# Kernel optimization log

Measured on AMD Instinct MI355X. Metric: run time of the kernel, lower is better.

Reference implementation:

```python
import jax, jax.numpy as jnp
import numpy as np

EPS = 1e-5
B, C1, C2, H, W = 8, 256, 256, 80, 80
C_ = C2 // 2
K = 3

def _bn(x, g, b, m, v):
    # inference-mode BatchNorm with given affine params / running stats
    return g * (x - m) * jax.lax.rsqrt(v + EPS) + b

def setup_inputs():
    key = jax.random.key(0)
    ks = jax.random.split(key, 18)
    rn = jax.random.normal
    ru = jax.random.uniform
    inp = {}
    inp['x'] = rn(ks[0], (B, C1, H, W), jnp.float32)
    # cv1: 1x1 conv (no bias) + BN
    inp['W1'] = rn(ks[1], (C_, C1), jnp.float32) * 0.05
    inp['g1'] = 1.0 + 0.1 * rn(ks[2], (C_,), jnp.float32)
    inp['b1'] = 0.1 * rn(ks[3], (C_,), jnp.float32)
    inp['m1'] = 0.1 * rn(ks[4], (C_,), jnp.float32)
    inp['v1'] = 0.5 + ru(ks[5], (C_,), jnp.float32)
    # RFAConv.get_weights: grouped 1x1 conv (groups=C_, 9->9 per group, with bias) + BN
    inp['Wg'] = rn(ks[6], (C_, K * K, K * K), jnp.float32) * 0.2
    inp['bg'] = 0.1 * rn(ks[7], (C_, K * K), jnp.float32)
    inp['gg'] = 1.0 + 0.1 * rn(ks[8], (C_, K * K), jnp.float32)
    inp['bgw'] = 0.1 * rn(ks[9], (C_, K * K), jnp.float32)
    inp['mg'] = 0.1 * rn(ks[10], (C_, K * K), jnp.float32)
    inp['vg'] = 0.5 + ru(ks[11], (C_, K * K), jnp.float32)
    # RFAConv.conv: kernel-3 stride-3 conv flattened to [C2, C_, 9], with bias; + BN
    inp['Wc'] = rn(ks[12], (C2, C_, K * K), jnp.float32) * 0.03
    inp['bc'] = 0.1 * rn(ks[13], (C2,), jnp.float32)
    inp['g2'] = 1.0 + 0.1 * rn(ks[14], (C2,), jnp.float32)
    inp['b2'] = 0.1 * rn(ks[15], (C2,), jnp.float32)
    inp['m2'] = 0.1 * rn(ks[16], (C2,), jnp.float32)
    inp['v2'] = 0.5 + ru(ks[17], (C2,), jnp.float32)
    return inp

def reference(x, W1, g1, b1, m1, v1, Wg, bg, gg, bgw, mg, vg, Wc, bc, g2, b2, m2, v2):
    # cv1: 1x1 conv + BN + SiLU
    h = jnp.einsum('oc,bchw->bohw', W1, x)
    h = _bn(h, g1[:, None, None], b1[:, None, None], m1[:, None, None], v1[:, None, None])
    h = jax.nn.silu(h)
    # nn.Unfold(k=3, pad=1): patches[b, c, n, y, x] with n = i*3 + j (torch layout)
    hp = jnp.pad(h, ((0, 0), (0, 0), (1, 1), (1, 1)))
    patches = jnp.stack([hp[:, :, i:i + H, j:j + W] for i in range(K) for j in range(K)], axis=2)  # [B,C_,9,H,W]
    # grouped 1x1 conv (per-channel 9->9 mixing) + BN + softmax over receptive field
    w = jnp.einsum('coi,bcihw->bcohw', Wg, patches) + bg[:, :, None, None]
    w = _bn(w, gg[:, :, None, None], bgw[:, :, None, None], mg[:, :, None, None], vg[:, :, None, None])
    w = jax.nn.softmax(w, axis=2)
    # weighted receptive-field data; stride-3 kernel-3 conv over the block-expanded
    # (3H,3W) layout reduces exactly to a contraction over (channel, kernel-index)
    out = jnp.einsum('ocn,bcnhw->bohw', Wc, patches * w) + bc[:, None, None]
    out = _bn(out, g2[:, None, None], b2[:, None, None], m2[:, None, None], v2[:, None, None])
    out = jax.nn.relu(out)
    return x + out
```

## Files before the change

kernel.cpp:

```cpp
#include <hip/hip_runtime.h>
#include <hip/hip_bf16.h>

#define B_   8
#define C1_  256
#define C2_  256
#define Cm_  128
#define H_   80
#define W_   80
#define HW_  6400
#define CN_  1152
#define EPS_ 1e-5f

typedef __attribute__((ext_vector_type(8))) short bf16x8;
typedef __attribute__((ext_vector_type(4))) float f32x4;

__device__ inline unsigned short f2bf(float f) {
  union { float f; unsigned int u; } v; v.f = f;
  unsigned int u = v.u;
  unsigned int r = (u + 0x7FFFu + ((u >> 16) & 1u)) >> 16;
  return (unsigned short)r;
}
__device__ inline float bf2f(unsigned short s) {
  union { unsigned int u; float f; } v; v.u = ((unsigned int)s) << 16;
  return v.f;
}

__device__ __forceinline__ void gload16(const void* g, void* l) {
  __builtin_amdgcn_global_load_lds(
      (const __attribute__((address_space(1))) void*)g,
      (__attribute__((address_space(3))) void*)l, 16, 0, 0);
}

__global__ __launch_bounds__(256) void k0_prep(
    const float* __restrict__ Wc, const float* __restrict__ bc,
    const float* __restrict__ g2, const float* __restrict__ b2,
    const float* __restrict__ m2, const float* __restrict__ v2,
    const float* __restrict__ Wg, const float* __restrict__ bg,
    const float* __restrict__ gg, const float* __restrict__ bgw,
    const float* __restrict__ mg, const float* __restrict__ vg,
    const float* __restrict__ W1,
    unsigned short* __restrict__ Wcb, float* __restrict__ A2,
    float* __restrict__ B2, float* __restrict__ Wgt,
    float* __restrict__ bgt, unsigned short* __restrict__ W1b) {
  int idx = blockIdx.x * 256 + threadIdx.x;
  if (idx < C2_ * CN_) {
    int o = idx / CN_;
    int r = idx - o * CN_;
    int n = r >> 7;
    int c = r & 127;
    Wcb[idx] = f2bf(Wc[o * CN_ + c * 9 + n]);
  }
  if (idx < Cm_ * 81) {
    int c  = idx / 81;
    int oi = idx - c * 81;
    int n  = oi / 9;
    float sg = gg[c * 9 + n] * rsqrtf(vg[c * 9 + n] + EPS_);
    Wgt[oi * 128 + c] = Wg[idx] * sg;
  }
  if (idx < Cm_ * 9) {
    int c = idx / 9;
    int n = idx - c * 9;
    float sg = gg[idx] * rsqrtf(vg[idx] + EPS_);
    bgt[n * 128 + c] = (bg[idx] - mg[idx]) * sg + bgw[idx];
  }
  if (idx < Cm_ * C1_) W1b[idx] = f2bf(W1[idx]);
  if (idx < C2_) {
    float s = g2[idx] * rsqrtf(v2[idx] + EPS_);
    A2[idx] = s;
    B2[idx] = (bc[idx] - m2[idx]) * s + b2[idx];
  }
}

__global__ __launch_bounds__(256) void k1_cv1(
    const float* __restrict__ x, const unsigned short* __restrict__ W1b,
    const float* __restrict__ g1, const float* __restrict__ b1,
    const float* __restrict__ m1, const float* __restrict__ v1,
    unsigned short* __restrict__ h) {
  __shared__ alignas(16) unsigned short Ash[2][128 * 64];
  __shared__ alignas(16) unsigned short Bsh[2][64 * 64];

  const int b   = blockIdx.y;
  const int hw0 = blockIdx.x * 64;
  const int t   = threadIdx.x;
  const int w   = __builtin_amdgcn_readfirstlane(t >> 6);
  const int l15 = t & 15;
  const int lhi = (t & 63) >> 4;

  const char* W1B = (const char*)W1b;
  int aoffs[4], aldsb[4];
#pragma unroll
  for (int j = 0; j < 4; ++j) {
    int L16  = j * 256 + t;
    int row  = L16 >> 3;
    int colb = (L16 & 7) * 16;
    aoffs[j] = row * (C1_ * 2) + (colb ^ ((row & 7) << 4));
    aldsb[j] = L16 * 16;
  }
  const int c_l = t & 63;
  const int px0 = (t >> 6) * 16;

#define STAGEA(BUF, KC)                                                        \
  _Pragma("unroll") for (int j = 0; j < 4; ++j)                                \
      gload16(W1B + aoffs[j] + (KC) * 128, (char*)&Ash[BUF][0] + aldsb[j]);
#define LOADB(KC)                                                              \
  _Pragma("unroll") for (int u = 0; u < 4; ++u)                                \
      xv[u] = *reinterpret_cast<const float4*>(                                \
          x + ((size_t)(b * C1_ + (KC) * 64 + c_l)) * HW_ + hw0 + px0 + u * 4);
#define WRITEB(BUF)                                                            \
  _Pragma("unroll") for (int u = 0; u < 4; ++u)                                \
    _Pragma("unroll") for (int e = 0; e < 4; ++e) {                            \
      int px = px0 + u * 4 + e;                                                \
      float vv = (e == 0) ? xv[u].x : (e == 1) ? xv[u].y                       \
               : (e == 2) ? xv[u].z : xv[u].w;                                 \
      Bsh[BUF][px * 64 + (c_l ^ (((u * 4 + e) & 7) << 3))] = f2bf(vv);         \
    }

  f32x4 acc[2][4];
#pragma unroll
  for (int i = 0; i < 2; ++i)
#pragma unroll
    for (int nf = 0; nf < 4; ++nf) acc[i][nf] = (f32x4)0.f;

  const int swzs = (l15 & 7) << 3;
  const int lhi8 = lhi * 8;

  float4 xv[4];
  STAGEA(0, 0);
  LOADB(0);
  WRITEB(0);
  __syncthreads();

  int cur = 0;
  for (int kc = 0; kc < 4; ++kc) {
    if (kc < 3) {
      STAGEA(cur ^ 1, kc + 1);
      LOADB(kc + 1);
    }
    const unsigned short* Ab = &Ash[cur][0];
    const unsigned short* Bb = &Bsh[cur][0];
#pragma unroll
    for (int ks = 0; ks < 2; ++ks) {
      bf16x8 av[2], bv[4];
#pragma unroll
      for (int mf = 0; mf < 2; ++mf) {
        int row = w * 32 + mf * 16 + l15;
        av[mf] = *reinterpret_cast<const bf16x8*>(
            Ab + row * 64 + (((ks << 5) + lhi8) ^ swzs));
      }
#pragma unroll
      for (int nf = 0; nf < 4; ++nf) {
        int row = nf * 16 + l15;
        bv[nf] = *reinterpret_cast<const bf16x8*>(
            Bb + row * 64 + (((ks << 5) + lhi8) ^ swzs));
      }
#pragma unroll
      for (int mf = 0; mf < 2; ++mf)
#pragma unroll
        for (int nf = 0; nf < 4; ++nf)
          acc[mf][nf] = __builtin_amdgcn_mfma_f32_16x16x32_bf16(
              av[mf], bv[nf], acc[mf][nf], 0, 0, 0);
    }
    if (kc < 3) WRITEB(cur ^ 1);
    __syncthreads();
    cur ^= 1;
  }
#undef STAGEA
#undef LOADB
#undef WRITEB

#pragma unroll
  for (int mf = 0; mf < 2; ++mf) {
#pragma unroll
    for (int r = 0; r < 4; ++r) {
      int o = w * 32 + mf * 16 + lhi * 4 + r;
      float s  = g1[o] * rsqrtf(v1[o] + EPS_);
      float sh = b1[o] - m1[o] * s;
#pragma unroll
      for (int nf = 0; nf < 4; ++nf) {
        float val = fmaf(acc[mf][nf][r], s, sh);
        float sig = 1.f / (1.f + __expf(-val));
        h[((size_t)b * Cm_ + o) * HW_ + hw0 + nf * 16 + l15] = f2bf(val * sig);
      }
    }
  }
}

__global__ __launch_bounds__(256) void k2a_weights(
    const unsigned short* __restrict__ h,
    const float* __restrict__ Wgt, const float* __restrict__ bgt,
    unsigned short* __restrict__ vt) {
  __shared__ unsigned short ht[Cm_ * 30];
  __shared__ unsigned short vbuf[8][CN_];

  const int b  = blockIdx.z;
  const int y  = blockIdx.y;
  const int x0 = blockIdx.x * 8;
  const int t  = threadIdx.x;

  for (int idx = t; idx < Cm_ * 30; idx += 256) {
    int c   = idx / 30;
    int rem = idx - c * 30;
    int r   = rem / 10;
    int xx  = rem - r * 10;
    int gy  = y + r - 1;
    int gx  = x0 + xx - 1;
    unsigned short val = 0;
    if ((unsigned)gy < (unsigned)H_ && (unsigned)gx < (unsigned)W_)
      val = h[((size_t)b * Cm_ + c) * HW_ + gy * W_ + gx];
    ht[idx] = val;
  }
  __syncthreads();

  const int c  = t & 127;
  const int p0 = t >> 7;

  float p[4][9];
  {
    float f[3][10];
#pragma unroll
    for (int r = 0; r < 3; ++r) {
      const unsigned int* src =
          reinterpret_cast<const unsigned int*>(&ht[c * 30 + r * 10]);
#pragma unroll
      for (int u = 0; u < 5; ++u) {
        unsigned int d = src[u];
        f[r][2 * u]     = bf2f((unsigned short)(d & 0xffffu));
        f[r][2 * u + 1] = bf2f((unsigned short)(d >> 16));
      }
    }
#pragma unroll
    for (int j = 0; j < 4; ++j)
#pragma unroll
      for (int r = 0; r < 3; ++r)
#pragma unroll
        for (int cc = 0; cc < 3; ++cc)
          p[j][r * 3 + cc] = p0 ? f[r][2 * j + 1 + cc] : f[r][2 * j + cc];
  }

  float wv[9][4];
#pragma unroll
  for (int n = 0; n < 9; ++n) {
    float bgv = bgt[n * 128 + c];
    float wg[9];
#pragma unroll
    for (int i = 0; i < 9; ++i) wg[i] = Wgt[(n * 9 + i) * 128 + c];
#pragma unroll
    for (int j = 0; j < 4; ++j) {
      float a = bgv;
#pragma unroll
      for (int i = 0; i < 9; ++i) a = fmaf(wg[i], p[j][i], a);
      wv[n][j] = a;
    }
  }

#pragma unroll
  for (int j = 0; j < 4; ++j) {
    int px = p0 + 2 * j;
    float mx = wv[0][j];
#pragma unroll
    for (int n = 1; n < 9; ++n) mx = fmaxf(mx, wv[n][j]);
    float e[9], sum = 0.f;
#pragma unroll
    for (int n = 0; n < 9; ++n) { e[n] = __expf(wv[n][j] - mx); sum += e[n]; }
    float inv = 1.f / sum;
#pragma unroll
    for (int n = 0; n < 9; ++n)
      vbuf[px][n * 128 + c] = f2bf(p[j][n] * e[n] * inv);
  }
  __syncthreads();

  for (int idx = t; idx < 8 * (CN_ / 8); idx += 256) {
    int px  = idx / 144;
    int off = idx - px * 144;
    const uint4* src = reinterpret_cast<const uint4*>(&vbuf[px][off * 8]);
    int hw = y * W_ + x0 + px;
    uint4* dst = reinterpret_cast<uint4*>(vt + ((size_t)b * HW_ + hw) * CN_ + off * 8);
    *dst = *src;
  }
}

__global__ __launch_bounds__(512, 4) void k2b_gemm(
    const unsigned short* __restrict__ Wcb, const unsigned short* __restrict__ vt,
    const float* __restrict__ A2, const float* __restrict__ B2,
    const float* __restrict__ x, float* __restrict__ out) {
  __shared__ alignas(16) unsigned short Ash[2][256 * 64];
  __shared__ alignas(16) unsigned short Bsh[2][64 * 64];

  const int b   = blockIdx.y;
  const int n0  = blockIdx.x * 64;
  const int t   = threadIdx.x;
  const int w   = __builtin_amdgcn_readfirstlane(t >> 6);
  const int l   = t & 63;
  const int l15 = l & 15;
  const int lhi = l >> 4;
  const int mw  = w >> 1;
  const int nw  = w & 1;

  const char* WcbB = (const char*)Wcb;
  const char* vtB  = (const char*)vt;
  int  aoffs[4], aldsb[4];
#pragma unroll
  for (int j = 0; j < 4; ++j) {
    int L16  = (w * 4 + j) * 64 + l;
    int row  = L16 >> 3;
    int colb = (L16 & 7) * 16;
    aoffs[j] = row * (CN_ * 2) + (colb ^ ((row & 7) << 4));
    aldsb[j] = L16 * 16;
  }
  const int bpx  = t >> 3;
  const long boff = (long)((size_t)(b * HW_ + n0 + bpx) * CN_) * 2 +
                    (((t & 7) * 16) ^ ((bpx & 7) << 4));
  const int bldsb = t * 16;

#define STAGE(BUF, TT) do {                                                    \
    _Pragma("unroll") for (int j = 0; j < 4; ++j)                              \
      gload16(WcbB + aoffs[j] + (TT) * 128, (char*)&Ash[BUF][0] + aldsb[j]);   \
    gload16(vtB + boff + (TT) * 128, (char*)&Bsh[BUF][0] + bldsb);             \
  } while (0)

  f32x4 acc[4][2];
#pragma unroll
  for (int i = 0; i < 4; ++i)
#pragma unroll
    for (int nf = 0; nf < 2; ++nf) acc[i][nf] = (f32x4)0.f;

  const int swzs = (l15 & 7) << 3;
  const int lhi8 = lhi * 8;

  STAGE(0, 0);
  __syncthreads();

  int cur = 0;
  for (int tt = 0; tt < 18; ++tt) {
    if (tt < 17) STAGE(cur ^ 1, tt + 1);
    const unsigned short* Ab = &Ash[cur][0];
    const unsigned short* Bb = &Bsh[cur][0];
#pragma unroll
    for (int ks = 0; ks < 2; ++ks) {
      bf16x8 av[4], bv[2];
#pragma unroll
      for (int mf = 0; mf < 4; ++mf) {
        int row = mw * 64 + mf * 16 + l15;
        av[mf] = *reinterpret_cast<const bf16x8*>(
            Ab + row * 64 + (((ks << 5) + lhi8) ^ swzs));
      }
#pragma unroll
      for (int nf = 0; nf < 2; ++nf) {
        int row = nw * 32 + nf * 16 + l15;
        bv[nf] = *reinterpret_cast<const bf16x8*>(
            Bb + row * 64 + (((ks << 5) + lhi8) ^ swzs));
      }
#pragma unroll
      for (int mf = 0; mf < 4; ++mf)
#pragma unroll
        for (int nf = 0; nf < 2; ++nf)
          acc[mf][nf] = __builtin_amdgcn_mfma_f32_16x16x32_bf16(
              av[mf], bv[nf], acc[mf][nf], 0, 0, 0);
    }
    __syncthreads();
    cur ^= 1;
  }
#undef STAGE

#pragma unroll
  for (int mf = 0; mf < 4; ++mf) {
#pragma unroll
    for (int r = 0; r < 4; ++r) {
      int o = mw * 64 + mf * 16 + lhi * 4 + r;
      float sA = A2[o], sB = B2[o];
#pragma unroll
      for (int nf = 0; nf < 2; ++nf) {
        float val = fmaf(acc[mf][nf][r], sA, sB);
        val = fmaxf(val, 0.f);
        size_t idx = ((size_t)b * C2_ + o) * HW_ + n0 + nw * 32 + nf * 16 + l15;
        out[idx] = x[idx] + val;
      }
    }
  }
}

extern "C" void kernel_launch(void* const* d_in, const int* in_sizes, int n_in,
                              void* d_out, int out_size, void* d_ws, size_t ws_size,
                              hipStream_t stream) {
  (void)in_sizes; (void)n_in; (void)out_size; (void)ws_size;
  const float* x   = (const float*)d_in[0];
  const float* W1  = (const float*)d_in[1];
  const float* g1  = (const float*)d_in[2];
  const float* b1  = (const float*)d_in[3];
  const float* m1  = (const float*)d_in[4];
  const float* v1  = (const float*)d_in[5];
  const float* Wg  = (const float*)d_in[6];
  const float* bg  = (const float*)d_in[7];
  const float* gg  = (const float*)d_in[8];
  const float* bgw = (const float*)d_in[9];
  const float* mg  = (const float*)d_in[10];
  const float* vg  = (const float*)d_in[11];
  const float* Wc  = (const float*)d_in[12];
  const float* bc  = (const float*)d_in[13];
  const float* g2  = (const float*)d_in[14];
  const float* b2  = (const float*)d_in[15];
  const float* m2  = (const float*)d_in[16];
  const float* v2  = (const float*)d_in[17];
  float* outp = (float*)d_out;

  char* ws = (char*)d_ws;
  unsigned short* h   = (unsigned short*)ws;
  unsigned short* vt  = (unsigned short*)(ws + 13107200);
  unsigned short* Wcb = (unsigned short*)(ws + 131072000);
  float*          Wgt = (float*)(ws + 131661824);
  float*          bgt = (float*)(ws + 131703296);
  float*          A2  = (float*)(ws + 131707904);
  float*          B2  = A2 + C2_;
  unsigned short* W1b = (unsigned short*)(ws + 131709952);

  k0_prep<<<dim3((C2_ * CN_ + 255) / 256), 256, 0, stream>>>(
      Wc, bc, g2, b2, m2, v2, Wg, bg, gg, bgw, mg, vg, W1,
      Wcb, A2, B2, Wgt, bgt, W1b);

  dim3 grid1(HW_ / 64, B_);
  k1_cv1<<<grid1, 256, 0, stream>>>(x, W1b, g1, b1, m1, v1, h);

  dim3 grid2a(W_ / 8, H_, B_);
  k2a_weights<<<grid2a, 256, 0, stream>>>(h, Wgt, bgt, vt);

  dim3 grid2b(HW_ / 64, B_);
  k2b_gemm<<<grid2b, 512, 0, stream>>>(Wcb, vt, A2, B2, x, outp);
}
```

Before: 152.7 us.

## Fuse receptive-field attention weighting into the output GEMM, removing vt intermediate

Merges the softmax-weighting kernel and the output GEMM into one kernel. Each block handles 40 pixels of one row, computes the weighted patches for 32-channel chunks into shared memory, and immediately runs MFMAs against Wc read directly from global memory. This removes the roughly 118 MB bf16 vt round-trip through HBM, and Wc is now used in its natural (c, n) ordering. The cost is that A operands are no longer staged through LDS. Using 48 N-columns for 40 pixels wastes some MFMA work, and the vbuf layout may cause LDS bank conflicts.

New measurement: 232.4 us. +52.3%, slower.

```diff
diff --git a/kernel.cpp b/kernel.cpp
--- a/kernel.cpp
+++ b/kernel.cpp
@@ -10,6 +10,12 @@
 #define HW_  6400
 #define CN_  1152
 #define EPS_ 1e-5f
+
+#define CH_   32
+#define NCHK_ 4
+#define KCH_  288
+#define NPX_  40
+#define VSTR_ 296
 
 typedef __attribute__((ext_vector_type(8))) short bf16x8;
 typedef __attribute__((ext_vector_type(4))) float f32x4;
@@ -43,13 +49,7 @@
     float* __restrict__ B2, float* __restrict__ Wgt,
     float* __restrict__ bgt, unsigned short* __restrict__ W1b) {
   int idx = blockIdx.x * 256 + threadIdx.x;
-  if (idx < C2_ * CN_) {
-    int o = idx / CN_;
-    int r = idx - o * CN_;
-    int n = r >> 7;
-    int c = r & 127;
-    Wcb[idx] = f2bf(Wc[o * CN_ + c * 9 + n]);
-  }
+  if (idx < C2_ * CN_) Wcb[idx] = f2bf(Wc[idx]);
   if (idx < Cm_ * 81) {
     int c  = idx / 81;
     int oi = idx - c * 81;
@@ -185,195 +185,134 @@
   }
 }
 
-__global__ __launch_bounds__(256) void k2a_weights(
+__global__ __launch_bounds__(256, 2) void k2f(
     const unsigned short* __restrict__ h,
     const float* __restrict__ Wgt, const float* __restrict__ bgt,
-    unsigned short* __restrict__ vt) {
-  __shared__ unsigned short ht[Cm_ * 30];
-  __shared__ unsigned short vbuf[8][CN_];
-
-  const int b  = blockIdx.z;
-  const int y  = blockIdx.y;
-  const int x0 = blockIdx.x * 8;
-  const int t  = threadIdx.x;
-
-  for (int idx = t; idx < Cm_ * 30; idx += 256) {
-    int c   = idx / 30;
-    int rem = idx - c * 30;
-    int r   = rem / 10;
-    int xx  = rem - r * 10;
-    int gy  = y + r - 1;
-    int gx  = x0 + xx - 1;
-    unsigned short val = 0;
-    if ((unsigned)gy < (unsigned)H_ && (unsigned)gx < (unsigned)W_)
-      val = h[((size_t)b * Cm_ + c) * HW_ + gy * W_ + gx];
-    ht[idx] = val;
-  }
-  __syncthreads();
-
-  const int c  = t & 127;
-  const int p0 = t >> 7;
-
-  float p[4][9];
-  {
-    float f[3][10];
-#pragma unroll
-    for (int r = 0; r < 3; ++r) {
-      const unsigned int* src =
-          reinterpret_cast<const unsigned int*>(&ht[c * 30 + r * 10]);
-#pragma unroll
-      for (int u = 0; u < 5; ++u) {
-        unsigned int d = src[u];
-        f[r][2 * u]     = bf2f((unsigned short)(d & 0xffffu));
-        f[r][2 * u + 1] = bf2f((unsigned short)(d >> 16));
-      }
-    }
-#pragma unroll
-    for (int j = 0; j < 4; ++j)
-#pragma unroll
-      for (int r = 0; r < 3; ++r)
-#pragma unroll
-        for (int cc = 0; cc < 3; ++cc)
-          p[j][r * 3 + cc] = p0 ? f[r][2 * j + 1 + cc] : f[r][2 * j + cc];
-  }
-
-  float wv[9][4];
-#pragma unroll
-  for (int n = 0; n < 9; ++n) {
-    float bgv = bgt[n * 128 + c];
-    float wg[9];
-#pragma unroll
-    for (int i = 0; i < 9; ++i) wg[i] = Wgt[(n * 9 + i) * 128 + c];
-#pragma unroll
-    for (int j = 0; j < 4; ++j) {
-      float a = bgv;
-#pragma unroll
-      for (int i = 0; i < 9; ++i) a = fmaf(wg[i], p[j][i], a);
-      wv[n][j] = a;
-    }
-  }
-
-#pragma unroll
-  for (int j = 0; j < 4; ++j) {
-    int px = p0 + 2 * j;
-    float mx = wv[0][j];
-#pragma unroll
-    for (int n = 1; n < 9; ++n) mx = fmaxf(mx, wv[n][j]);
-    float e[9], sum = 0.f;
-#pragma unroll
-    for (int n = 0; n < 9; ++n) { e[n] = __expf(wv[n][j] - mx); sum += e[n]; }
-    float inv = 1.f / sum;
-#pragma unroll
-    for (int n = 0; n < 9; ++n)
-      vbuf[px][n * 128 + c] = f2bf(p[j][n] * e[n] * inv);
-  }
-  __syncthreads();
-
-  for (int idx = t; idx < 8 * (CN_ / 8); idx += 256) {
-    int px  = idx / 144;
-    int off = idx - px * 144;
-    const uint4* src = reinterpret_cast<const uint4*>(&vbuf[px][off * 8]);
-    int hw = y * W_ + x0 + px;
-    uint4* dst = reinterpret_cast<uint4*>(vt + ((size_t)b * HW_ + hw) * CN_ + off * 8);
-    *dst = *src;
-  }
-}
-
-__global__ __launch_bounds__(512, 4) void k2b_gemm(
-    const unsigned short* __restrict__ Wcb, const unsigned short* __restrict__ vt,
+    const unsigned short* __restrict__ Wcb,
     const float* __restrict__ A2, const float* __restrict__ B2,
     const float* __restrict__ x, float* __restrict__ out) {
-  __shared__ alignas(16) unsigned short Ash[2][256 * 64];
-  __shared__ alignas(16) unsigned short Bsh[2][64 * 64];
-
-  const int b   = blockIdx.y;
-  const int n0  = blockIdx.x * 64;
-  const int t   = threadIdx.x;
-  const int w   = __builtin_amdgcn_readfirstlane(t >> 6);
-  const int l   = t & 63;
-  const int l15 = l & 15;
-  const int lhi = l >> 4;
-  const int mw  = w >> 1;
-  const int nw  = w & 1;
-
-  const char* WcbB = (const char*)Wcb;
-  const char* vtB  = (const char*)vt;
-  int  aoffs[4], aldsb[4];
-#pragma unroll
-  for (int j = 0; j < 4; ++j) {
-    int L16  = (w * 4 + j) * 64 + l;
-    int row  = L16 >> 3;
-    int colb = (L16 & 7) * 16;
-    aoffs[j] = row * (CN_ * 2) + (colb ^ ((row & 7) << 4));
-    aldsb[j] = L16 * 16;
-  }
-  const int bpx  = t >> 3;
-  const long boff = (long)((size_t)(b * HW_ + n0 + bpx) * CN_) * 2 +
-                    (((t & 7) * 16) ^ ((bpx & 7) << 4));
-  const int bldsb = t * 16;
-
-#define STAGE(BUF, TT) do {                                                    \
-    _Pragma("unroll") for (int j = 0; j < 4; ++j)                              \
-      gload16(WcbB + aoffs[j] + (TT) * 128, (char*)&Ash[BUF][0] + aldsb[j]);   \
-    gload16(vtB + boff + (TT) * 128, (char*)&Bsh[BUF][0] + bldsb);             \
-  } while (0)
-
-  f32x4 acc[4][2];
-#pragma unroll
-  for (int i = 0; i < 4; ++i)
-#pragma unroll
-    for (int nf = 0; nf < 2; ++nf) acc[i][nf] = (f32x4)0.f;
-
-  const int swzs = (l15 & 7) << 3;
-  const int lhi8 = lhi * 8;
-
-  STAGE(0, 0);
-  __syncthreads();
-
-  int cur = 0;
-  for (int tt = 0; tt < 18; ++tt) {
-    if (tt < 17) STAGE(cur ^ 1, tt + 1);
-    const unsigned short* Ab = &Ash[cur][0];
-    const unsigned short* Bb = &Bsh[cur][0];
-#pragma unroll
-    for (int ks = 0; ks < 2; ++ks) {
-      bf16x8 av[4], bv[2];
-#pragma unroll
-      for (int mf = 0; mf < 4; ++mf) {
-        int row = mw * 64 + mf * 16 + l15;
+  __shared__ unsigned short ht[CH_ * 3 * 42];
+  __shared__ alignas(16) unsigned short vbuf[48 * VSTR_];
+
+  const int half = blockIdx.x;
+  const int y    = blockIdx.y;
+  const int b    = blockIdx.z;
+  const int x0   = half * NPX_;
+  const int t    = threadIdx.x;
+  const int w    = __builtin_amdgcn_readfirstlane(t >> 6);
+  const int l15  = t & 15;
+  const int lhi  = (t & 63) >> 4;
+
+  const int c_l = t & 31;
+  const int pxg = t >> 5;
+
+  f32x4 acc[4][3];
+#pragma unroll
+  for (int mf = 0; mf < 4; ++mf)
+#pragma unroll
+    for (int nf = 0; nf < 3; ++nf) acc[mf][nf] = (f32x4)0.f;
+
+  for (int ch = 0; ch < NCHK_; ++ch) {
+#pragma unroll
+    for (int i = 0; i < 16; ++i) {
+      int idx = t + i * 256;
+      if (idx < CH_ * 3 * 42) {
+        int c   = idx / 126;
+        int rem = idx - c * 126;
+        int r   = rem / 42;
+        int xx  = rem - r * 42;
+        int gy  = y + r - 1;
+        int gx  = x0 + xx - 1;
+        unsigned short v = 0;
+        if ((unsigned)gy < (unsigned)H_ && (unsigned)gx < (unsigned)W_)
+          v = h[((size_t)b * Cm_ + ch * CH_ + c) * HW_ + gy * W_ + gx];
+        ht[idx] = v;
+      }
+    }
+    __syncthreads();
+
+    {
+      float f[3][7];
+      const int fb = c_l * 126 + pxg * 5;
+#pragma unroll
+      for (int r = 0; r < 3; ++r)
+#pragma unroll
+        for (int q = 0; q < 7; ++q)
+          f[r][q] = bf2f(ht[fb + r * 42 + q]);
+
+      const int cg = ch * CH_ + c_l;
+      float wv[9][5];
+#pragma unroll
+      for (int n = 0; n < 9; ++n) {
+        float bias = bgt[n * 128 + cg];
+        float wg[9];
+#pragma unroll
+        for (int i = 0; i < 9; ++i) wg[i] = Wgt[(n * 9 + i) * 128 + cg];
+#pragma unroll
+        for (int j = 0; j < 5; ++j) {
+          float a = bias;
+#pragma unroll
+          for (int ri = 0; ri < 3; ++ri)
+#pragma unroll
+            for (int ci = 0; ci < 3; ++ci)
+              a = fmaf(wg[ri * 3 + ci], f[ri][j + ci], a);
+          wv[n][j] = a;
+        }
+      }
+#pragma unroll
+      for (int j = 0; j < 5; ++j) {
+        float mx = wv[0][j];
+#pragma unroll
+        for (int n = 1; n < 9; ++n) mx = fmaxf(mx, wv[n][j]);
+        float e[9], sum = 0.f;
+#pragma unroll
+        for (int n = 0; n < 9; ++n) { e[n] = __expf(wv[n][j] - mx); sum += e[n]; }
+        float inv = 1.f / sum;
+        int vb = (pxg * 5 + j) * VSTR_ + c_l * 9;
+#pragma unroll
+        for (int n = 0; n < 9; ++n)
+          vbuf[vb + n] = f2bf(f[n / 3][j + n % 3] * e[n] * inv);
+      }
+    }
+    __syncthreads();
+
+#pragma unroll
+    for (int ks = 0; ks < 9; ++ks) {
+      bf16x8 av[4], bv[3];
+#pragma unroll
+      for (int mf = 0; mf < 4; ++mf)
         av[mf] = *reinterpret_cast<const bf16x8*>(
-            Ab + row * 64 + (((ks << 5) + lhi8) ^ swzs));
-      }
-#pragma unroll
-      for (int nf = 0; nf < 2; ++nf) {
-        int row = nw * 32 + nf * 16 + l15;
+            Wcb + (size_t)(w * 64 + mf * 16 + l15) * CN_ +
+            ch * KCH_ + ks * 32 + lhi * 8);
+#pragma unroll
+      for (int nf = 0; nf < 3; ++nf)
         bv[nf] = *reinterpret_cast<const bf16x8*>(
-            Bb + row * 64 + (((ks << 5) + lhi8) ^ swzs));
-      }
+            vbuf + (nf * 16 + l15) * VSTR_ + ks * 32 + lhi * 8);
 #pragma unroll
       for (int mf = 0; mf < 4; ++mf)
 #pragma unroll
-        for (int nf = 0; nf < 2; ++nf)
+        for (int nf = 0; nf < 3; ++nf)
           acc[mf][nf] = __builtin_amdgcn_mfma_f32_16x16x32_bf16(
               av[mf], bv[nf], acc[mf][nf], 0, 0, 0);
     }
     __syncthreads();
-    cur ^= 1;
-  }
-#undef STAGE
+  }
 
 #pragma unroll
   for (int mf = 0; mf < 4; ++mf) {
 #pragma unroll
     for (int r = 0; r < 4; ++r) {
-      int o = mw * 64 + mf * 16 + lhi * 4 + r;
+      int o = w * 64 + mf * 16 + lhi * 4 + r;
       float sA = A2[o], sB = B2[o];
 #pragma unroll
-      for (int nf = 0; nf < 2; ++nf) {
-        float val = fmaf(acc[mf][nf][r], sA, sB);
-        val = fmaxf(val, 0.f);
-        size_t idx = ((size_t)b * C2_ + o) * HW_ + n0 + nw * 32 + nf * 16 + l15;
-        out[idx] = x[idx] + val;
+      for (int nf = 0; nf < 3; ++nf) {
+        int px = nf * 16 + l15;
+        if (px < NPX_) {
+          float val = fmaf(acc[mf][nf][r], sA, sB);
+          val = fmaxf(val, 0.f);
+          size_t idx = ((size_t)b * C2_ + o) * HW_ + y * W_ + x0 + px;
+          out[idx] = x[idx] + val;
+        }
       }
     }
   }
@@ -405,13 +344,12 @@
 
   char* ws = (char*)d_ws;
   unsigned short* h   = (unsigned short*)ws;
-  unsigned short* vt  = (unsigned short*)(ws + 13107200);
-  unsigned short* Wcb = (unsigned short*)(ws + 131072000);
-  float*          Wgt = (float*)(ws + 131661824);
-  float*          bgt = (float*)(ws + 131703296);
-  float*          A2  = (float*)(ws + 131707904);
+  unsigned short* Wcb = (unsigned short*)(ws + 13107200);
+  float*          Wgt = (float*)(ws + 13697024);
+  float*          bgt = (float*)(ws + 13738496);
+  float*          A2  = (float*)(ws + 13743104);
   float*          B2  = A2 + C2_;
-  unsigned short* W1b = (unsigned short*)(ws + 131709952);
+  unsigned short* W1b = (unsigned short*)(ws + 13745152);
 
   k0_prep<<<dim3((C2_ * CN_ + 255) / 256), 256, 0, stream>>>(
       Wc, bc, g2, b2, m2, v2, Wg, bg, gg, bgw, mg, vg, W1,
@@ -420,9 +358,6 @@
   dim3 grid1(HW_ / 64, B_);
   k1_cv1<<<grid1, 256, 0, stream>>>(x, W1b, g1, b1, m1, v1, h);
 
-  dim3 grid2a(W_ / 8, H_, B_);
-  k2a_weights<<<grid2a, 256, 0, stream>>>(h, Wgt, bgt, vt);
-
-  dim3 grid2b(HW_ / 64, B_);
-  k2b_gemm<<<grid2b, 512, 0, stream>>>(Wcb, vt, A2, B2, x, outp);
-}
+  dim3 grid2(2, H_, B_);
+  k2f<<<grid2, 256, 0, stream>>>(h, Wgt, bgt, Wcb, A2, B2, x, outp);
+}
```

## Write softmax-weighted patches directly to global, drop LDS staging buffer

Applied to the files above, without the earlier changes.

The weights kernel now gives each thread two adjacent channels and two pixels instead of one channel and four pixels. Weights and biases are read as float2, and the bf16-packed results are stored straight to global memory as 32-bit words. This removes the vbuf shared staging array, one barrier and the 16-byte copy-out loop, which cuts LDS usage and may raise occupancy. In exchange the global stores become 4-byte writes rather than 16-byte vector stores, and rounding now goes through the HIP bf16 intrinsic.

New measurement: 184.3 us. 20.7% more time.

```diff
diff --git a/kernel.cpp b/kernel.cpp
--- a/kernel.cpp
+++ b/kernel.cpp
@@ -23,6 +23,11 @@
 __device__ inline float bf2f(unsigned short s) {
   union { unsigned int u; float f; } v; v.u = ((unsigned int)s) << 16;
   return v.f;
+}
+__device__ inline unsigned short bfb(float f) {
+  __hip_bfloat16 b = __float2bfloat16(f);
+  union { __hip_bfloat16 b; unsigned short u; } v; v.b = b;
+  return v.u;
 }
 
 __device__ __forceinline__ void gload16(const void* g, void* l) {
@@ -190,7 +195,6 @@
     const float* __restrict__ Wgt, const float* __restrict__ bgt,
     unsigned short* __restrict__ vt) {
   __shared__ unsigned short ht[Cm_ * 30];
-  __shared__ unsigned short vbuf[8][CN_];
 
   const int b  = blockIdx.z;
   const int y  = blockIdx.y;
@@ -211,71 +215,71 @@
   }
   __syncthreads();
 
-  const int c  = t & 127;
-  const int p0 = t >> 7;
-
-  float p[4][9];
-  {
-    float f[3][10];
+  const int cp = t & 63;
+  const int pp = t >> 6;
+
+  float f[2][3][4];
+#pragma unroll
+  for (int ch = 0; ch < 2; ++ch) {
+    int c = cp * 2 + ch;
 #pragma unroll
     for (int r = 0; r < 3; ++r) {
       const unsigned int* src =
-          reinterpret_cast<const unsigned int*>(&ht[c * 30 + r * 10]);
-#pragma unroll
-      for (int u = 0; u < 5; ++u) {
-        unsigned int d = src[u];
-        f[r][2 * u]     = bf2f((unsigned short)(d & 0xffffu));
-        f[r][2 * u + 1] = bf2f((unsigned short)(d >> 16));
-      }
-    }
-#pragma unroll
-    for (int j = 0; j < 4; ++j)
-#pragma unroll
-      for (int r = 0; r < 3; ++r)
-#pragma unroll
-        for (int cc = 0; cc < 3; ++cc)
-          p[j][r * 3 + cc] = p0 ? f[r][2 * j + 1 + cc] : f[r][2 * j + cc];
-  }
-
-  float wv[9][4];
+          reinterpret_cast<const unsigned int*>(&ht[c * 30 + r * 10]) + pp;
+      unsigned int d0 = src[0], d1 = src[1];
+      f[ch][r][0] = bf2f((unsigned short)(d0 & 0xffffu));
+      f[ch][r][1] = bf2f((unsigned short)(d0 >> 16));
+      f[ch][r][2] = bf2f((unsigned short)(d1 & 0xffffu));
+      f[ch][r][3] = bf2f((unsigned short)(d1 >> 16));
+    }
+  }
+
+  const float2* Wg2 = (const float2*)Wgt;
+  const float2* bg2 = (const float2*)bgt;
+
+  float wv[9][2][2];
 #pragma unroll
   for (int n = 0; n < 9; ++n) {
-    float bgv = bgt[n * 128 + c];
-    float wg[9];
-#pragma unroll
-    for (int i = 0; i < 9; ++i) wg[i] = Wgt[(n * 9 + i) * 128 + c];
-#pragma unroll
-    for (int j = 0; j < 4; ++j) {
-      float a = bgv;
-#pragma unroll
-      for (int i = 0; i < 9; ++i) a = fmaf(wg[i], p[j][i], a);
-      wv[n][j] = a;
-    }
-  }
-
-#pragma unroll
-  for (int j = 0; j < 4; ++j) {
-    int px = p0 + 2 * j;
-    float mx = wv[0][j];
-#pragma unroll
-    for (int n = 1; n < 9; ++n) mx = fmaxf(mx, wv[n][j]);
-    float e[9], sum = 0.f;
-#pragma unroll
-    for (int n = 0; n < 9; ++n) { e[n] = __expf(wv[n][j] - mx); sum += e[n]; }
-    float inv = 1.f / sum;
-#pragma unroll
-    for (int n = 0; n < 9; ++n)
-      vbuf[px][n * 128 + c] = f2bf(p[j][n] * e[n] * inv);
-  }
-  __syncthreads();
-
-  for (int idx = t; idx < 8 * (CN_ / 8); idx += 256) {
-    int px  = idx / 144;
-    int off = idx - px * 144;
-    const uint4* src = reinterpret_cast<const uint4*>(&vbuf[px][off * 8]);
-    int hw = y * W_ + x0 + px;
-    uint4* dst = reinterpret_cast<uint4*>(vt + ((size_t)b * HW_ + hw) * CN_ + off * 8);
-    *dst = *src;
+    float2 bias = bg2[n * 64 + cp];
+    float a00 = bias.x, a01 = bias.x, a10 = bias.y, a11 = bias.y;
+#pragma unroll
+    for (int ri = 0; ri < 3; ++ri)
+#pragma unroll
+      for (int ci = 0; ci < 3; ++ci) {
+        float2 wgi = Wg2[(n * 9 + ri * 3 + ci) * 64 + cp];
+        a00 = fmaf(wgi.x, f[0][ri][0 + ci], a00);
+        a01 = fmaf(wgi.x, f[0][ri][1 + ci], a01);
+        a10 = fmaf(wgi.y, f[1][ri][0 + ci], a10);
+        a11 = fmaf(wgi.y, f[1][ri][1 + ci], a11);
+      }
+    wv[n][0][0] = a00; wv[n][0][1] = a01;
+    wv[n][1][0] = a10; wv[n][1][1] = a11;
+  }
+
+#pragma unroll
+  for (int jj = 0; jj < 2; ++jj) {
+    int px = 2 * pp + jj;
+    float mx0 = wv[0][0][jj], mx1 = wv[0][1][jj];
+#pragma unroll
+    for (int n = 1; n < 9; ++n) {
+      mx0 = fmaxf(mx0, wv[n][0][jj]);
+      mx1 = fmaxf(mx1, wv[n][1][jj]);
+    }
+    float e0[9], e1[9], s0 = 0.f, s1 = 0.f;
+#pragma unroll
+    for (int n = 0; n < 9; ++n) {
+      e0[n] = __expf(wv[n][0][jj] - mx0); s0 += e0[n];
+      e1[n] = __expf(wv[n][1][jj] - mx1); s1 += e1[n];
+    }
+    float i0 = 1.f / s0, i1 = 1.f / s1;
+    size_t base = ((size_t)(b * HW_ + y * W_ + x0 + px)) * CN_ + 2 * cp;
+#pragma unroll
+    for (int n = 0; n < 9; ++n) {
+      float v0 = f[0][n / 3][jj + n % 3] * e0[n] * i0;
+      float v1 = f[1][n / 3][jj + n % 3] * e1[n] * i1;
+      unsigned int pk = ((unsigned int)bfb(v1) << 16) | bfb(v0);
+      *reinterpret_cast<unsigned int*>(vt + base + n * 128) = pk;
+    }
   }
 }
 
```
